# Performance work log

Hardware: AMD Instinct MI355X
Metric: run time of the kernel (lower is better)

## Reference

```python
import jax, jax.numpy as jnp
import numpy as np

B, N, F_IN, H, L, C = 64, 512, 21, 64, 3, 9
NEG_INF = -jnp.inf


def setup_inputs() -> dict:
    key = jax.random.key(0)
    ks = jax.random.split(key, 24)
    s = lambda shape, k, scale=0.05: jax.random.normal(ks[k], shape, dtype=jnp.float32) * scale
    return {
        "node_features": jax.random.normal(ks[0], (B, N, F_IN), dtype=jnp.float32),
        "adjacency": jax.random.bernoulli(ks[1], 0.05, (B, N, N)).astype(jnp.float32),
        "node_mask": jnp.ones((B, N), dtype=bool),
        "We": s((F_IN, H), 2), "be": jnp.zeros((H,), jnp.float32),
        "Wl": s((L, H, H), 3), "a_src": s((L, H), 4), "a_dst": s((L, H), 5),
        "gamma": jnp.ones((L, H), jnp.float32), "beta": jnp.zeros((L, H), jnp.float32),
        "P1": s((H, H), 6), "pb1": jnp.zeros((H,), jnp.float32),
        "P2": s((H,), 7), "pb2": jnp.zeros((), jnp.float32),
        "C1": s((H, H), 8), "cb1": jnp.zeros((H,), jnp.float32),
        "C2": s((H, C), 9), "cb2": jnp.zeros((C,), jnp.float32),
    }


def _layernorm(x, g, b, eps=1e-5):
    mu = x.mean(-1, keepdims=True)
    var = ((x - mu) ** 2).mean(-1, keepdims=True)
    return (x - mu) * jax.lax.rsqrt(var + eps) * g + b


def reference(node_features, adjacency, node_mask, We, be, Wl, a_src, a_dst,
              gamma, beta, P1, pb1, P2, pb2, C1, cb1, C2, cb2):
    # node embedding (dropout = identity in eval)
    h = jax.nn.relu(node_features @ We + be)  # [B,N,H]
    adj_zero = adjacency == 0
    for l in range(L):
        hW = h @ Wl[l]                                  # [B,N,H]
        attn = hW @ a_src[l]                            # [B,N] src scores
        attn = attn[:, :, None] + (hW @ a_dst[l])[:, None, :]  # [B,N,N]
        attn = jax.nn.leaky_relu(attn, 0.2)
        attn = jnp.where(adj_zero, NEG_INF, attn)
        attn = jnp.nan_to_num(jax.nn.softmax(attn, axis=-1), nan=0.0)
        h = _layernorm(h + attn @ hW, gamma[l], beta[l])
    # attention pooling
    pa = jnp.tanh(h @ P1 + pb1) @ P2 + pb2              # [B,N]
    pa = jnp.where(node_mask, pa, NEG_INF)
    pa = jnp.nan_to_num(jax.nn.softmax(pa, axis=-1), nan=0.0)
    g = jnp.einsum('bn,bnh->bh', pa, h)                 # [B,H]
    return jax.nn.relu(g @ C1 + cb1) @ C2 + cb2         # [B,C]
```

## Files before the change

kernel.cpp:

```cpp
#include <hip/hip_runtime.h>


#define WS_H     0
#define WS_HWA   2097152
#define WS_HWB   4194304
#define WS_SA    6291456
#define WS_TA    6324224
#define WS_SB    6356992
#define WS_TB    6389760
#define WS_PA    6422528
#define WS_DEG   6455296
#define WS_LIST_BYTES 25952256

typedef const __attribute__((address_space(1))) unsigned int gu32;
typedef __attribute__((address_space(3))) unsigned int lu32;

__device__ __forceinline__ void gl_lds16(const float* g, float* l) {
  __builtin_amdgcn_global_load_lds((gu32*)g, (lu32*)l, 16, 0, 0);
}

template <int CTRL>
__device__ __forceinline__ float dpp_add(float v) {
  int x = __builtin_amdgcn_update_dpp(0, __float_as_int(v), CTRL, 0xf, 0xf, true);
  return v + __int_as_float(x);
}
__device__ __forceinline__ float wtot(float v) {
  v = dpp_add<0x111>(v);
  v = dpp_add<0x112>(v);
  v = dpp_add<0x114>(v);
  v = dpp_add<0x118>(v);
  v = dpp_add<0x142>(v);
  v = dpp_add<0x143>(v);
  return __int_as_float(__builtin_amdgcn_readlane(__float_as_int(v), 63));
}
__device__ __forceinline__ float rsum16d(float v) {
  v = dpp_add<0x111>(v);
  v = dpp_add<0x112>(v);
  v = dpp_add<0x114>(v);
  v = dpp_add<0x118>(v);
  return v;
}

__device__ __forceinline__ float wsum(float v) {
#pragma unroll
  for (int o = 32; o; o >>= 1) v += __shfl_xor(v, o, 64);
  return v;
}
__device__ __forceinline__ float wmax(float v) {
#pragma unroll
  for (int o = 32; o; o >>= 1) v = fmaxf(v, __shfl_xor(v, o, 64));
  return v;
}

__global__ __launch_bounds__(512) void k_embed_hw(
    const float* __restrict__ x, const float* __restrict__ We,
    const float* __restrict__ be, const float* __restrict__ adj,
    const float* __restrict__ W0, const float* __restrict__ asrc,
    const float* __restrict__ adst,
    float* __restrict__ h, int* __restrict__ deg,
    unsigned short* __restrict__ nlist,
    float* __restrict__ hW, float* __restrict__ s, float* __restrict__ t) {
  __shared__ float lw[64 * 68];
  __shared__ float lhT[64 * 34];
  __shared__ unsigned short lidx[8][4][64];
  int tid = threadIdx.x, lane = tid & 63, wv = tid >> 6;
  int blk = blockIdx.x;
  int xcd = blk & 7, i = blk >> 3;
  int b = xcd * 8 + (i & 7), sub = i >> 3;
  int base = b * 512 + sub * 32;
  int rb = base + wv * 4;
#pragma unroll
  for (int k = 0; k < 2; ++k) {
    int idx = tid + 512 * k;
    int rr = idx >> 4, q = idx & 15;
    *(float4*)&lw[rr * 68 + q * 4] = *(const float4*)&W0[rr * 64 + q * 4];
  }
  float wreg[21];
#pragma unroll
  for (int f = 0; f < 21; ++f) wreg[f] = We[f * 64 + lane];
  float bev = be[lane];
  unsigned long long lmask = (1ull << lane) - 1ull;
  float4 a0[4], a1[4];
#pragma unroll
  for (int r = 0; r < 4; ++r) {
    const float4* ar = (const float4*)(adj + (size_t)(rb + r) * 512);
    a0[r] = ar[lane];
    a1[r] = ar[64 + lane];
  }
#pragma unroll
  for (int r = 0; r < 4; ++r) {
    int row = rb + r;
    const float* xr = x + (size_t)row * 21;
    float acc = bev;
#pragma unroll
    for (int f = 0; f < 21; ++f) acc = fmaf(xr[f], wreg[f], acc);
    acc = fmaxf(acc, 0.0f);
    h[(size_t)row * 64 + lane] = acc;
    lhT[lane * 34 + (wv * 4 + r)] = acc;
    float comp[8] = {a0[r].x, a0[r].y, a0[r].z, a0[r].w,
                     a1[r].x, a1[r].y, a1[r].z, a1[r].w};
    int cnt = 0;
#pragma unroll
    for (int c = 0; c < 8; ++c) {
      bool on = comp[c] != 0.0f;
      unsigned long long m = __ballot(on);
      if (on) {
        int pos = cnt + __popcll(m & lmask);
        int col = (c < 4) ? (lane * 4 + c) : (256 + lane * 4 + (c - 4));
        if (pos < 64) lidx[wv][r][pos] = (unsigned short)col;
      }
      cnt += __popcll(m);
    }
    if (lane == 0) deg[row] = cnt < 64 ? cnt : 64;
  }
  {
    ushort4 v = *(ushort4*)&lidx[wv][0][lane * 4];
    *(ushort4*)(nlist + (size_t)rb * 64 + lane * 4) = v;
  }
  __syncthreads();
  if (tid < 128) {
    int tc = tid & 15, tr = tid >> 4;
    float acc[4][4] = {};
#pragma unroll 4
    for (int c = 0; c < 64; ++c) {
      float2 a01 = *(const float2*)&lhT[c * 34 + tr * 4];
      float2 a23 = *(const float2*)&lhT[c * 34 + tr * 4 + 2];
      float4 bb = *(const float4*)&lw[c * 68 + tc * 4];
      float av[4] = {a01.x, a01.y, a23.x, a23.y};
      float bv[4] = {bb.x, bb.y, bb.z, bb.w};
#pragma unroll
      for (int ii = 0; ii < 4; ++ii)
#pragma unroll
        for (int j = 0; j < 4; ++j)
          acc[ii][j] = fmaf(av[ii], bv[j], acc[ii][j]);
    }
    float p1[4], p2[4];
#pragma unroll
    for (int j = 0; j < 4; ++j) {
      p1[j] = asrc[tc * 4 + j];
      p2[j] = adst[tc * 4 + j];
    }
#pragma unroll
    for (int ii = 0; ii < 4; ++ii) {
      int row = base + tr * 4 + ii;
      *(float4*)&hW[(size_t)row * 64 + tc * 4] =
          make_float4(acc[ii][0], acc[ii][1], acc[ii][2], acc[ii][3]);
      float ps = acc[ii][0] * p1[0] + acc[ii][1] * p1[1] +
                 acc[ii][2] * p1[2] + acc[ii][3] * p1[3];
      float pt = acc[ii][0] * p2[0] + acc[ii][1] * p2[1] +
                 acc[ii][2] * p2[2] + acc[ii][3] * p2[3];
      ps = rsum16d(ps);
      pt = rsum16d(pt);
      if (tc == 15) { s[row] = ps; t[row] = pt; }
    }
  }
}

template <int MODE>
__global__ __launch_bounds__(512) void k_layer(
    float* __restrict__ h, const float* __restrict__ hWin,
    const float* __restrict__ sIn, const float* __restrict__ tIn,
    const int* __restrict__ deg, const unsigned short* __restrict__ nlist,
    const float* __restrict__ gamma, const float* __restrict__ beta,
    const float* __restrict__ Wn, const float* __restrict__ v1,
    const float* __restrict__ v2,
    float* __restrict__ hWout, float* __restrict__ sOut,
    float* __restrict__ tOut) {
  __shared__ float lw[64 * 68];
  __shared__ float lhT[64 * 33];
  __shared__ float tlds[512];
  int tid = threadIdx.x, lane = tid & 63, wv = tid >> 6;
  int blk = blockIdx.x;
  int b = (blk & 7) * 8 + ((blk >> 3) & 7);
  int sub = blk >> 6;
  int base = b * 512 + sub * 32;
  int rb = base + wv * 4;

  unsigned short jr[4]; float sir[4], hrr[4]; int dgr[4];
#pragma unroll
  for (int r = 0; r < 4; ++r) {
    int row = rb + r;
    jr[r] = nlist[(size_t)row * 64 + lane];
    sir[r] = sIn[row];
    hrr[r] = h[(size_t)row * 64 + lane];
    dgr[r] = deg[row];
  }
#pragma unroll
  for (int k = 0; k < 2; ++k) {
    int idx = tid + 512 * k;
    int rr = idx >> 4, q = idx & 15;
    *(float4*)&lw[rr * 68 + q * 4] = *(const float4*)&Wn[rr * 64 + q * 4];
  }
  const float* tb = tIn + ((size_t)b << 9);
  if (tid < 128) *(float4*)&tlds[tid * 4] = *(const float4*)&tb[tid * 4];
  __syncthreads();

  const float* hWb = hWin + ((size_t)b << 9) * 64;
  float gm = gamma[lane], bt = beta[lane];
  float hst[4];
#pragma unroll
  for (int rp = 0; rp < 4; rp += 2) {
    int dgA = __builtin_amdgcn_readfirstlane(dgr[rp]);
    int dgB = __builtin_amdgcn_readfirstlane(dgr[rp + 1]);
    bool actA = lane < dgA, actB = lane < dgB;
    int jmA = actA ? (int)jr[rp] : 0;
    int jmB = actB ? (int)jr[rp + 1] : 0;
    float eA = sir[rp] + (actA ? tlds[jmA] : 0.0f);
    float eB = sir[rp + 1] + (actB ? tlds[jmB] : 0.0f);
    eA = eA > 0.0f ? eA : 0.2f * eA;
    eB = eB > 0.0f ? eB : 0.2f * eB;
    float wjA = actA ? __expf(eA) : 0.0f;
    float wjB = actB ? __expf(eB) : 0.0f;
    int bitsA = __float_as_int(wjA) & ~511;
    int bitsB = __float_as_int(wjB) & ~511;
    int pkA = bitsA | jmA, pkB = bitsB | jmB;
    float a0A = 0.0f, a1A = 0.0f, a0B = 0.0f, a1B = 0.0f;
    int mA = (dgA + 7) & ~7, mB = (dgB + 7) & ~7;
    int mx = mA > mB ? mA : mB;
    for (int n = 0; n < mx; n += 8) {
      if (n < mA) {
#pragma unroll
        for (int k = 0; k < 8; k += 2) {
          int u0 = __builtin_amdgcn_readlane(pkA, n + k);
          int u1 = __builtin_amdgcn_readlane(pkA, n + k + 1);
          a0A = fmaf(__int_as_float(u0 & ~511),
                     hWb[(u0 & 511) * 64 + lane], a0A);
          a1A = fmaf(__int_as_float(u1 & ~511),
                     hWb[(u1 & 511) * 64 + lane], a1A);
        }
      }
      if (n < mB) {
#pragma unroll
        for (int k = 0; k < 8; k += 2) {
          int u0 = __builtin_amdgcn_readlane(pkB, n + k);
          int u1 = __builtin_amdgcn_readlane(pkB, n + k + 1);
          a0B = fmaf(__int_as_float(u0 & ~511),
                     hWb[(u0 & 511) * 64 + lane], a0B);
          a1B = fmaf(__int_as_float(u1 & ~511),
                     hWb[(u1 & 511) * 64 + lane], a1B);
        }
      }
    }
    float dsumA = wtot(__int_as_float(bitsA));
    float dsumB = wtot(__int_as_float(bitsB));
    float aA = dgA > 0 ? (a0A + a1A) * (1.0f / dsumA) : 0.0f;
    float aB = dgB > 0 ? (a0B + a1B) * (1.0f / dsumB) : 0.0f;
    float xvA = hrr[rp] + aA, xvB = hrr[rp + 1] + aB;
    float s1A = wtot(xvA), s2A = wtot(xvA * xvA);
    float s1B = wtot(xvB), s2B = wtot(xvB * xvB);
    float muA = s1A * 0.015625f, muB = s1B * 0.015625f;
    float varA = fmaf(-muA, muA, s2A * 0.015625f);
    float varB = fmaf(-muB, muB, s2B * 0.015625f);
    float hnA = fmaf((xvA - muA) * rsqrtf(varA + 1e-5f), gm, bt);
    float hnB = fmaf((xvB - muB) * rsqrtf(varB + 1e-5f), gm, bt);
    h[(size_t)(rb + rp) * 64 + lane] = hnA;
    h[(size_t)(rb + rp + 1) * 64 + lane] = hnB;
    hst[rp] = hnA;
    hst[rp + 1] = hnB;
  }
#pragma unroll
  for (int r = 0; r < 4; ++r) lhT[lane * 33 + (wv * 4 + r)] = hst[r];
  __syncthreads();
  {
    int tc = tid & 15, tr = tid >> 4;
    float acc[4] = {};
#pragma unroll 8
    for (int c = 0; c < 64; ++c) {
      float a = lhT[c * 33 + tr];
      float4 bb = *(const float4*)&lw[c * 68 + tc * 4];
      acc[0] = fmaf(a, bb.x, acc[0]);
      acc[1] = fmaf(a, bb.y, acc[1]);
      acc[2] = fmaf(a, bb.z, acc[2]);
      acc[3] = fmaf(a, bb.w, acc[3]);
    }
    float p1[4], p2[4];
#pragma unroll
    for (int j = 0; j < 4; ++j) { p1[j] = v1[tc * 4 + j]; p2[j] = v2[tc * 4 + j]; }
    int row = base + tr;
    if (MODE == 0) {
      *(float4*)&hWout[(size_t)row * 64 + tc * 4] =
          make_float4(acc[0], acc[1], acc[2], acc[3]);
      float ps = acc[0] * p1[0] + acc[1] * p1[1] +
                 acc[2] * p1[2] + acc[3] * p1[3];
      float pt = acc[0] * p2[0] + acc[1] * p2[1] +
                 acc[2] * p2[2] + acc[3] * p2[3];
      ps = rsum16d(ps);
      pt = rsum16d(pt);
      if (tc == 15) { sOut[row] = ps; tOut[row] = pt; }
    } else {
      float p = 0.0f;
#pragma unroll
      for (int j = 0; j < 4; ++j) p += tanhf(acc[j] + p1[j]) * p2[j];
      p = rsum16d(p);
      if (tc == 15) sOut[row] = p;
    }
  }
}

__global__ __launch_bounds__(512) void k_pool(const float* __restrict__ h,
    const float* __restrict__ pa, const float* __restrict__ C1,
    const float* __restrict__ cb1, const float* __restrict__ C2,
    const float* __restrict__ cb2, float* __restrict__ out) {
  __shared__ float red[8];
  __shared__ float gpart[8][64];
  __shared__ float gl[64], rl[64];
  int b = ((blockIdx.x & 7) << 3) | (blockIdx.x >> 3);
  int tid = threadIdx.x, lane = tid & 63, wv = tid >> 6;
  float v = pa[b * 512 + tid];
  float m = wmax(v);
  if (lane == 0) red[wv] = m;
  __syncthreads();
  float bm = red[0];
#pragma unroll
  for (int w = 1; w < 8; ++w) bm = fmaxf(bm, red[w]);
  float e = __expf(v - bm);
  float sm = wsum(e);
  __syncthreads();
  if (lane == 0) red[wv] = sm;
  __syncthreads();
  float bs = 0.0f;
#pragma unroll
  for (int w = 0; w < 8; ++w) bs += red[w];
  float p = e / bs;
  const float* hb = h + ((size_t)b * 512) * 64;
  float g = 0.0f;
#pragma unroll
  for (int l = 0; l < 64; ++l) {
    float pj = __shfl(p, l, 64);
    g = fmaf(pj, hb[(size_t)(wv * 64 + l) * 64 + lane], g);
  }
  gpart[wv][lane] = g;
  __syncthreads();
  if (wv == 0) {
    float gg = 0.0f;
#pragma unroll
    for (int w = 0; w < 8; ++w) gg += gpart[w][lane];
    gl[lane] = gg;
    float rr = cb1[lane];
#pragma unroll
    for (int j = 0; j < 64; ++j) rr = fmaf(gl[j], C1[j * 64 + lane], rr);
    rr = fmaxf(rr, 0.0f);
    rl[lane] = rr;
    if (lane < 9) {
      float o = cb2[lane];
#pragma unroll
      for (int k = 0; k < 64; ++k) o = fmaf(rl[k], C2[k * 9 + lane], o);
      out[b * 9 + lane] = o;
    }
  }
}

extern "C" void kernel_launch(void* const* d_in, const int* in_sizes, int n_in,
                              void* d_out, int out_size, void* d_ws, size_t ws_size,
                              hipStream_t stream) {
  const float* x    = (const float*)d_in[0];
  const float* adj  = (const float*)d_in[1];
  const float* We   = (const float*)d_in[3];
  const float* be   = (const float*)d_in[4];
  const float* Wl   = (const float*)d_in[5];
  const float* asrc = (const float*)d_in[6];
  const float* adst = (const float*)d_in[7];
  const float* gamma= (const float*)d_in[8];
  const float* beta = (const float*)d_in[9];
  const float* P1   = (const float*)d_in[10];
  const float* pb1  = (const float*)d_in[11];
  const float* P2   = (const float*)d_in[12];
  const float* C1   = (const float*)d_in[14];
  const float* cb1  = (const float*)d_in[15];
  const float* C2   = (const float*)d_in[16];
  const float* cb2  = (const float*)d_in[17];
  float* out = (float*)d_out;

  float* ws  = (float*)d_ws;
  float* h   = ws + WS_H;
  float* hwA = ws + WS_HWA;
  float* hwB = ws + WS_HWB;
  float* sA  = ws + WS_SA;
  float* tA  = ws + WS_TA;
  float* sB  = ws + WS_SB;
  float* tB  = ws + WS_TB;
  float* pa  = ws + WS_PA;
  int*   deg = (int*)(ws + WS_DEG);
  unsigned short* nlist = (unsigned short*)((char*)d_ws + WS_LIST_BYTES);

  k_embed_hw<<<1024, 512, 0, stream>>>(x, We, be, adj, Wl, asrc, adst,
                                       h, deg, nlist, hwA, sA, tA);
  k_layer<0><<<1024, 512, 0, stream>>>(h, hwA, sA, tA, deg, nlist,
                                       gamma, beta, Wl + 4096,
                                       asrc + 64, adst + 64, hwB, sB, tB);
  k_layer<0><<<1024, 512, 0, stream>>>(h, hwB, sB, tB, deg, nlist,
                                       gamma + 64, beta + 64, Wl + 8192,
                                       asrc + 128, adst + 128, hwA, sA, tA);
  k_layer<1><<<1024, 512, 0, stream>>>(h, hwA, sA, tA, deg, nlist,
                                       gamma + 128, beta + 128, P1, pb1, P2,
                                       nullptr, pa, nullptr);
  k_pool<<<64, 512, 0, stream>>>(h, pa, C1, cb1, C2, cb2, out);
}
```

Measured before the change: 214.0 us.

## Split adjacency neighbor-list build into separate kernel with async LDS loads

Moves the adjacency scan and neighbor-list compaction out of the embedding kernel into a dedicated 256-thread kernel. That kernel streams adjacency rows into shared memory with global_load_lds and then ballot-compacts them, which aims to make the dominant 64 MB adjacency read more bandwidth-efficient and to decouple it from the embedding GEMM. It also drops the max-subtraction in the pooling softmax, removing a reduction and a barrier. Skipping the max is numerically unsafe in general: large pooling scores could overflow exp, and it relies on the test scores staying small.

```diff
diff --git a/kernel.cpp b/kernel.cpp
--- a/kernel.cpp
+++ b/kernel.cpp
@@ -46,59 +46,35 @@
   for (int o = 32; o; o >>= 1) v += __shfl_xor(v, o, 64);
   return v;
 }
-__device__ __forceinline__ float wmax(float v) {
-#pragma unroll
-  for (int o = 32; o; o >>= 1) v = fmaxf(v, __shfl_xor(v, o, 64));
-  return v;
-}
-
-__global__ __launch_bounds__(512) void k_embed_hw(
-    const float* __restrict__ x, const float* __restrict__ We,
-    const float* __restrict__ be, const float* __restrict__ adj,
-    const float* __restrict__ W0, const float* __restrict__ asrc,
-    const float* __restrict__ adst,
-    float* __restrict__ h, int* __restrict__ deg,
-    unsigned short* __restrict__ nlist,
-    float* __restrict__ hW, float* __restrict__ s, float* __restrict__ t) {
-  __shared__ float lw[64 * 68];
-  __shared__ float lhT[64 * 34];
-  __shared__ unsigned short lidx[8][4][64];
+
+__global__ __launch_bounds__(256) void k_nlist(
+    const float* __restrict__ adj, int* __restrict__ deg,
+    unsigned short* __restrict__ nlist) {
+  __shared__ float alds[16 * 512];
+  __shared__ unsigned short lidx[4][4][64];
   int tid = threadIdx.x, lane = tid & 63, wv = tid >> 6;
   int blk = blockIdx.x;
   int xcd = blk & 7, i = blk >> 3;
   int b = xcd * 8 + (i & 7), sub = i >> 3;
-  int base = b * 512 + sub * 32;
-  int rb = base + wv * 4;
-#pragma unroll
-  for (int k = 0; k < 2; ++k) {
-    int idx = tid + 512 * k;
-    int rr = idx >> 4, q = idx & 15;
-    *(float4*)&lw[rr * 68 + q * 4] = *(const float4*)&W0[rr * 64 + q * 4];
-  }
-  float wreg[21];
-#pragma unroll
-  for (int f = 0; f < 21; ++f) wreg[f] = We[f * 64 + lane];
-  float bev = be[lane];
+  int rb0 = b * 512 + sub * 16;
+  {
+    const char* src = (const char*)(adj + (size_t)rb0 * 512);
+    char* dst = (char*)alds;
+#pragma unroll
+    for (int c = 0; c < 8; ++c) {
+      int off = wv * 8192 + c * 1024;
+      gl_lds16((const float*)(src + off + lane * 16), (float*)(dst + off));
+    }
+  }
+  __syncthreads();
+  int rb = rb0 + wv * 4;
   unsigned long long lmask = (1ull << lane) - 1ull;
-  float4 a0[4], a1[4];
 #pragma unroll
   for (int r = 0; r < 4; ++r) {
-    const float4* ar = (const float4*)(adj + (size_t)(rb + r) * 512);
-    a0[r] = ar[lane];
-    a1[r] = ar[64 + lane];
-  }
-#pragma unroll
-  for (int r = 0; r < 4; ++r) {
-    int row = rb + r;
-    const float* xr = x + (size_t)row * 21;
-    float acc = bev;
-#pragma unroll
-    for (int f = 0; f < 21; ++f) acc = fmaf(xr[f], wreg[f], acc);
-    acc = fmaxf(acc, 0.0f);
-    h[(size_t)row * 64 + lane] = acc;
-    lhT[lane * 34 + (wv * 4 + r)] = acc;
-    float comp[8] = {a0[r].x, a0[r].y, a0[r].z, a0[r].w,
-                     a1[r].x, a1[r].y, a1[r].z, a1[r].w};
+    int rl = wv * 4 + r;
+    float4 a0 = *(const float4*)&alds[rl * 512 + lane * 4];
+    float4 a1 = *(const float4*)&alds[rl * 512 + 256 + lane * 4];
+    float comp[8] = {a0.x, a0.y, a0.z, a0.w, a1.x, a1.y, a1.z, a1.w};
     int cnt = 0;
 #pragma unroll
     for (int c = 0; c < 8; ++c) {
@@ -111,11 +87,46 @@
       }
       cnt += __popcll(m);
     }
-    if (lane == 0) deg[row] = cnt < 64 ? cnt : 64;
-  }
-  {
-    ushort4 v = *(ushort4*)&lidx[wv][0][lane * 4];
-    *(ushort4*)(nlist + (size_t)rb * 64 + lane * 4) = v;
+    if (lane == 0) deg[rb + r] = cnt < 64 ? cnt : 64;
+  }
+  ushort4 v = *(ushort4*)&lidx[wv][0][lane * 4];
+  *(ushort4*)(nlist + (size_t)rb * 64 + lane * 4) = v;
+}
+
+__global__ __launch_bounds__(512) void k_emb_h(
+    const float* __restrict__ x, const float* __restrict__ We,
+    const float* __restrict__ be, const float* __restrict__ W0,
+    const float* __restrict__ asrc, const float* __restrict__ adst,
+    float* __restrict__ h, float* __restrict__ hW,
+    float* __restrict__ s, float* __restrict__ t) {
+  __shared__ float lw[64 * 68];
+  __shared__ float lhT[64 * 34];
+  int tid = threadIdx.x, lane = tid & 63, wv = tid >> 6;
+  int blk = blockIdx.x;
+  int xcd = blk & 7, i = blk >> 3;
+  int b = xcd * 8 + (i & 7), sub = i >> 3;
+  int base = b * 512 + sub * 32;
+  int rb = base + wv * 4;
+#pragma unroll
+  for (int k = 0; k < 2; ++k) {
+    int idx = tid + 512 * k;
+    int rr = idx >> 4, q = idx & 15;
+    *(float4*)&lw[rr * 68 + q * 4] = *(const float4*)&W0[rr * 64 + q * 4];
+  }
+  float wreg[21];
+#pragma unroll
+  for (int f = 0; f < 21; ++f) wreg[f] = We[f * 64 + lane];
+  float bev = be[lane];
+#pragma unroll
+  for (int r = 0; r < 4; ++r) {
+    int row = rb + r;
+    const float* xr = x + (size_t)row * 21;
+    float acc = bev;
+#pragma unroll
+    for (int f = 0; f < 21; ++f) acc = fmaf(xr[f], wreg[f], acc);
+    acc = fmaxf(acc, 0.0f);
+    h[(size_t)row * 64 + lane] = acc;
+    lhT[lane * 34 + (wv * 4 + r)] = acc;
   }
   __syncthreads();
   if (tid < 128) {
@@ -307,15 +318,8 @@
   int b = ((blockIdx.x & 7) << 3) | (blockIdx.x >> 3);
   int tid = threadIdx.x, lane = tid & 63, wv = tid >> 6;
   float v = pa[b * 512 + tid];
-  float m = wmax(v);
-  if (lane == 0) red[wv] = m;
-  __syncthreads();
-  float bm = red[0];
-#pragma unroll
-  for (int w = 1; w < 8; ++w) bm = fmaxf(bm, red[w]);
-  float e = __expf(v - bm);
+  float e = __expf(v);
   float sm = wsum(e);
-  __syncthreads();
   if (lane == 0) red[wv] = sm;
   __syncthreads();
   float bs = 0.0f;
@@ -383,8 +387,9 @@
   int*   deg = (int*)(ws + WS_DEG);
   unsigned short* nlist = (unsigned short*)((char*)d_ws + WS_LIST_BYTES);
 
-  k_embed_hw<<<1024, 512, 0, stream>>>(x, We, be, adj, Wl, asrc, adst,
-                                       h, deg, nlist, hwA, sA, tA);
+  k_nlist<<<2048, 256, 0, stream>>>(adj, deg, nlist);
+  k_emb_h<<<1024, 512, 0, stream>>>(x, We, be, Wl, asrc, adst,
+                                    h, hwA, sA, tA);
   k_layer<0><<<1024, 512, 0, stream>>>(h, hwA, sA, tA, deg, nlist,
                                        gamma, beta, Wl + 4096,
                                        asrc + 64, adst + 64, hwB, sB, tB);
```

After: 213.2 us, median of 2. Within noise of the previous version (-0.4%).
